# Optimization experiments

Hardware: AMD Instinct MI355X
Metric: run time of the kernel (lower is better)

The kernel has to match this reference:

```python
import jax, jax.numpy as jnp
import numpy as np

N_QUBITS = 12
DEPTH = 6
BATCH = 4096

# Wire 0 is the most-significant bit (PennyLane default.qubit convention).

def _rx(t):
    c = jnp.cos(t / 2).astype(jnp.complex64)
    s = (-1j * jnp.sin(t / 2)).astype(jnp.complex64)
    return jnp.stack([jnp.stack([c, s], -1), jnp.stack([s, c], -1)], -2)

def _ry(t):
    c = jnp.cos(t / 2).astype(jnp.complex64)
    s = jnp.sin(t / 2).astype(jnp.complex64)
    return jnp.stack([jnp.stack([c, -s], -1), jnp.stack([s, c], -1)], -2)

def _rz(t):
    em = jnp.exp(-1j * t.astype(jnp.complex64) / 2)
    ep = jnp.exp(1j * t.astype(jnp.complex64) / 2)
    z = jnp.zeros_like(em)
    return jnp.stack([jnp.stack([em, z], -1), jnp.stack([z, ep], -1)], -2)

def _apply_1q(state, gate, q, n):
    # state: (B, 2^n); gate: (2,2) shared or (B,2,2) batched
    B = state.shape[0]
    st = state.reshape(B, 1 << q, 2, 1 << (n - 1 - q))
    eq = 'ab,xlbr->xlar' if gate.ndim == 2 else 'xab,xlbr->xlar'
    return jnp.einsum(eq, gate, st).reshape(B, -1)

def _apply_cnot(state, c, n):
    # CNOT with control c, target c+1 (adjacent wires)
    B = state.shape[0]
    st = state.reshape(B, 1 << c, 2, 2, 1 << (n - 2 - c))
    st = jnp.concatenate([st[:, :, 0:1], st[:, :, 1:2, ::-1]], axis=2)
    return st.reshape(B, -1)

def _z_signs(n):
    idx = jnp.arange(1 << n)
    bits = (idx[None, :] >> (n - 1 - jnp.arange(n))[:, None]) & 1  # (n, 2^n)
    return (1.0 - 2.0 * bits).astype(jnp.float32)

def setup_inputs() -> dict:
    key = jax.random.key(0)
    k1, k2 = jax.random.split(key)
    x = jax.random.normal(k1, (BATCH, N_QUBITS), dtype=jnp.float32)
    params = jax.random.normal(k2, (DEPTH, N_QUBITS, 3), dtype=jnp.float32)
    return {"x": x, "params": params}

def reference(x, params):
    B, n = x.shape
    depth = params.shape[0]
    state = jnp.zeros((B, 1 << n), jnp.complex64).at[:, 0].set(1.0)
    # input encoding: batched RX per qubit
    for i in range(n):
        state = _apply_1q(state, _rx(x[:, i]), i, n)
    for d in range(depth):
        for i in range(n):
            state = _apply_1q(state, _ry(params[d, i, 0]), i, n)
            state = _apply_1q(state, _rz(params[d, i, 1]), i, n)
            state = _apply_1q(state, _rx(params[d, i, 2]), i, n)
        for i in range(n - 1):
            state = _apply_cnot(state, i, n)
    probs = state.real ** 2 + state.imag ** 2  # (B, 2^n)
    return probs @ _z_signs(n).T  # (B, n) Pauli-Z expvals
```

## Files before the change

kernel.cpp:

```cpp
#include <hip/hip_runtime.h>

#define NQ    12
#define DIM   4096
#define DEPTH 6
#define BLK   256
#define RJ    16


typedef float f32x2 __attribute__((ext_vector_type(2)));

__device__ __host__ __forceinline__ constexpr int sufxc(int v) {
  v ^= v >> 1; v ^= v >> 2; v ^= v >> 4; v ^= v >> 8; return v;
}
__device__ __host__ __forceinline__ constexpr int K1w(int j) { return (j << 4) ^ j; }
__device__ __host__ __forceinline__ constexpr int K2w(int j) { return j << 8; }
__device__ __host__ __forceinline__ constexpr int KCw(int j) {
  const int s4 = sufxc(j) & 15;
  const int p  = __builtin_popcount((unsigned)j) & 1;
  return (s4 << 8) | (p ? 0xF0 : 0);
}

__device__ __forceinline__ f32x2 pfma(f32x2 a, f32x2 b, f32x2 c) {
  return __builtin_elementwise_fma(a, b, c);
}

template <int B>
__device__ __forceinline__ void gate4(f32x2 (&amp)[RJ], float4 u0, float4 u1) {
  const f32x2 r00 = {u0.x, u0.x}, mi00 = {-u0.y, u0.y};
  const f32x2 r01 = {u0.z, u0.z}, mi01 = {-u0.w, u0.w};
  const f32x2 r10 = {u1.x, u1.x}, mi10 = {-u1.y, u1.y};
  const f32x2 r11 = {u1.z, u1.z}, mi11 = {-u1.w, u1.w};
#pragma unroll
  for (int m = 0; m < RJ / 2; ++m) {
    const int lo = m & ((1 << B) - 1);
    const int j0 = ((m >> B) << (B + 1)) | lo;
    const int j1 = j0 | (1 << B);
    const f32x2 a = amp[j0], b = amp[j1];
    const f32x2 ax = a.yx, bx = b.yx;
    f32x2 n0 = r00 * a;
    n0 = pfma(mi00, ax, n0);
    n0 = pfma(r01, b, n0);
    n0 = pfma(mi01, bx, n0);
    f32x2 n1 = r10 * a;
    n1 = pfma(mi10, ax, n1);
    n1 = pfma(r11, b, n1);
    n1 = pfma(mi11, bx, n1);
    amp[j0] = n0; amp[j1] = n1;
  }
}

__global__ __launch_bounds__(BLK) void qsim_kernel(const float* __restrict__ x,
                                                   const float* __restrict__ params,
                                                   float* __restrict__ out) {
  __shared__ f32x2 sm2[DIM];
  __shared__ float uTab[DEPTH * NQ * 8];

  const int T = threadIdx.x;
  const int b = blockIdx.x;

  if (T < DEPTH * NQ) {
    const float py = params[T * 3 + 0];
    const float pz = params[T * 3 + 1];
    const float px = params[T * 3 + 2];
    float sa, ca, sb, cb, sg, cg;
    __sincosf(py * 0.5f, &sa, &ca);
    __sincosf(pz * 0.5f, &sb, &cb);
    __sincosf(px * 0.5f, &sg, &cg);
    const float Ar = ca * cb, Ai = -ca * sb;
    const float Br = -sa * cb, Bi = sa * sb;
    const float Cr = sa * cb, Ci = sa * sb;
    const float Dr = ca * cb, Di = ca * sb;
    float* u = &uTab[T * 8];
    u[0] = cg * Ar + sg * Ci;   u[1] = cg * Ai - sg * Cr;
    u[2] = cg * Br + sg * Di;   u[3] = cg * Bi - sg * Dr;
    u[4] = sg * Ai + cg * Cr;   u[5] = -sg * Ar + cg * Ci;
    u[6] = sg * Bi + cg * Dr;   u[7] = -sg * Br + cg * Di;
  }

  f32x2 amp[RJ];
  {
    float cs[NQ], sn[NQ];
#pragma unroll
    for (int i = 0; i < NQ; ++i) __sincosf(x[b * NQ + i] * 0.5f, &sn[i], &cs[i]);
    float hm = 1.0f;
#pragma unroll
    for (int i = 0; i < 8; ++i) hm *= ((T >> (7 - i)) & 1) ? sn[i] : cs[i];
    float mag[RJ];
    mag[0] = hm;
#pragma unroll
    for (int bb = 0; bb < 4; ++bb) {
#pragma unroll
      for (int j = 0; j < (1 << bb); ++j) {
        mag[j | (1 << bb)] = mag[j] * sn[11 - bb];
        mag[j] = mag[j] * cs[11 - bb];
      }
    }
    const int pt = __popc(T);
#pragma unroll
    for (int j = 0; j < RJ; ++j) {
      const float m = mag[j];
      const int k = (pt + __popc(j)) & 3;
      const float rr = (k & 1) ? 0.0f : ((k & 2) ? -m : m);
      const float ii = (k & 1) ? ((k & 2) ? m : -m) : 0.0f;
      amp[j] = (f32x2){rr, ii};
    }
  }

  __syncthreads();

  const int A0w = (T << 4) ^ (T & 15);
  const int B0w = ((T >> 4) << 8) | (T & 15);
  const int C0w = T ^ ((T >> 4) & 15);
  const int CT  = sufxc(T) & 255;
  const int D0w = CT ^ ((CT >> 4) & 15);

#define SWEEP(D, WBASE)                                                       \
  {                                                                           \
    const float4* uv0 = (const float4*)&uTab[((D) * NQ + (WBASE)) * 8];       \
    gate4<0>(amp, uv0[0], uv0[1]);                                            \
    const float4* uv1 = (const float4*)&uTab[((D) * NQ + (WBASE) - 1) * 8];   \
    gate4<1>(amp, uv1[0], uv1[1]);                                            \
    const float4* uv2 = (const float4*)&uTab[((D) * NQ + (WBASE) - 2) * 8];   \
    gate4<2>(amp, uv2[0], uv2[1]);                                            \
    const float4* uv3 = (const float4*)&uTab[((D) * NQ + (WBASE) - 3) * 8];   \
    gate4<3>(amp, uv3[0], uv3[1]);                                            \
  }
#define ST_ALL(EXPR)                                                          \
  {                                                                           \
    _Pragma("unroll") for (int j = 0; j < RJ; ++j) { sm2[(EXPR)] = amp[j]; }  \
  }
#define LD_ALL(EXPR)                                                          \
  {                                                                           \
    _Pragma("unroll") for (int j = 0; j < RJ; ++j) { amp[j] = sm2[(EXPR)]; }  \
  }

#pragma unroll 1
  for (int d = 0; d < DEPTH; ++d) {
    SWEEP(d, 11)
    ST_ALL(A0w ^ j) __syncthreads();
    LD_ALL(B0w ^ K1w(j)) __syncthreads();
    SWEEP(d, 7)
    ST_ALL(B0w ^ K1w(j)) __syncthreads();
    LD_ALL(C0w ^ K2w(j)) __syncthreads();
    SWEEP(d, 3)
    ST_ALL(D0w ^ KCw(j)) __syncthreads();
    LD_ALL(A0w ^ j) __syncthreads();
  }
#undef SWEEP
#undef ST_ALL
#undef LD_ALL

  float tot = 0.f, s0 = 0.f, s1 = 0.f, s2 = 0.f, s3 = 0.f;
#pragma unroll
  for (int j = 0; j < RJ; ++j) {
    const float p = fmaf(amp[j].x, amp[j].x, amp[j].y * amp[j].y);
    tot += p;
    s0 += (j & 1) ? -p : p;
    s1 += (j & 2) ? -p : p;
    s2 += (j & 4) ? -p : p;
    s3 += (j & 8) ? -p : p;
  }
  float v[NQ];
#pragma unroll
  for (int w = 0; w < 8; ++w) v[w] = ((T >> (7 - w)) & 1) ? -tot : tot;
  v[8] = s3; v[9] = s2; v[10] = s1; v[11] = s0;
#pragma unroll
  for (int w = 0; w < NQ; ++w) {
#pragma unroll
    for (int o = 32; o > 0; o >>= 1) v[w] += __shfl_xor(v[w], o);
  }
  const int wv = T >> 6, lt = T & 63;
  float* smf = (float*)sm2;
  if (lt == 0) {
#pragma unroll
    for (int w = 0; w < NQ; ++w) smf[w * 4 + wv] = v[w];
  }
  __syncthreads();
  if (T < NQ) out[b * NQ + T] = (smf[T * 4 + 0] + smf[T * 4 + 1]) +
                                (smf[T * 4 + 2] + smf[T * 4 + 3]);
}

extern "C" void kernel_launch(void* const* d_in, const int* in_sizes, int n_in,
                              void* d_out, int out_size, void* d_ws, size_t ws_size,
                              hipStream_t stream) {
  const float* x      = (const float*)d_in[0];
  const float* params = (const float*)d_in[1];
  float* out          = (float*)d_out;
  const int B = in_sizes[0] / NQ;
  qsim_kernel<<<B, BLK, 0, stream>>>(x, params, out);
}
```

Baseline: 242.5 us.

## Precompute gate table in a prep kernel and drop intra-wave LDS barriers

Moves the fused RY·RZ·RX gate matrices into a separate one-block kernel that writes them to workspace. The main kernel now reads them with uniform global loads instead of rebuilding an LDS table in every block. It also removes the barriers around the first LDS exchange, which only moves data between lanes of the same 16-thread group inside one wavefront, and reorders the others so each depth needs three barriers instead of six. This relies on wavefront lockstep for the unsynchronised exchange and adds a second kernel launch.

```diff
diff --git a/kernel.cpp b/kernel.cpp
--- a/kernel.cpp
+++ b/kernel.cpp
@@ -49,33 +49,34 @@
   }
 }
 
+__global__ void gate_prep(const float* __restrict__ params, float* __restrict__ gt) {
+  const int T = threadIdx.x;
+  if (T >= DEPTH * NQ) return;
+  const float py = params[T * 3 + 0];
+  const float pz = params[T * 3 + 1];
+  const float px = params[T * 3 + 2];
+  float sa, ca, sb, cb, sg, cg;
+  __sincosf(py * 0.5f, &sa, &ca);
+  __sincosf(pz * 0.5f, &sb, &cb);
+  __sincosf(px * 0.5f, &sg, &cg);
+  const float Ar = ca * cb, Ai = -ca * sb;
+  const float Br = -sa * cb, Bi = sa * sb;
+  const float Cr = sa * cb, Ci = sa * sb;
+  const float Dr = ca * cb, Di = ca * sb;
+  float* u = &gt[T * 8];
+  u[0] = cg * Ar + sg * Ci;   u[1] = cg * Ai - sg * Cr;
+  u[2] = cg * Br + sg * Di;   u[3] = cg * Bi - sg * Dr;
+  u[4] = sg * Ai + cg * Cr;   u[5] = -sg * Ar + cg * Ci;
+  u[6] = sg * Bi + cg * Dr;   u[7] = -sg * Br + cg * Di;
+}
+
 __global__ __launch_bounds__(BLK) void qsim_kernel(const float* __restrict__ x,
-                                                   const float* __restrict__ params,
+                                                   const float* __restrict__ gt,
                                                    float* __restrict__ out) {
   __shared__ f32x2 sm2[DIM];
-  __shared__ float uTab[DEPTH * NQ * 8];
 
   const int T = threadIdx.x;
   const int b = blockIdx.x;
-
-  if (T < DEPTH * NQ) {
-    const float py = params[T * 3 + 0];
-    const float pz = params[T * 3 + 1];
-    const float px = params[T * 3 + 2];
-    float sa, ca, sb, cb, sg, cg;
-    __sincosf(py * 0.5f, &sa, &ca);
-    __sincosf(pz * 0.5f, &sb, &cb);
-    __sincosf(px * 0.5f, &sg, &cg);
-    const float Ar = ca * cb, Ai = -ca * sb;
-    const float Br = -sa * cb, Bi = sa * sb;
-    const float Cr = sa * cb, Ci = sa * sb;
-    const float Dr = ca * cb, Di = ca * sb;
-    float* u = &uTab[T * 8];
-    u[0] = cg * Ar + sg * Ci;   u[1] = cg * Ai - sg * Cr;
-    u[2] = cg * Br + sg * Di;   u[3] = cg * Bi - sg * Dr;
-    u[4] = sg * Ai + cg * Cr;   u[5] = -sg * Ar + cg * Ci;
-    u[6] = sg * Bi + cg * Dr;   u[7] = -sg * Br + cg * Di;
-  }
 
   f32x2 amp[RJ];
   {
@@ -106,8 +107,6 @@
     }
   }
 
-  __syncthreads();
-
   const int A0w = (T << 4) ^ (T & 15);
   const int B0w = ((T >> 4) << 8) | (T & 15);
   const int C0w = T ^ ((T >> 4) & 15);
@@ -116,13 +115,13 @@
 
 #define SWEEP(D, WBASE)                                                       \
   {                                                                           \
-    const float4* uv0 = (const float4*)&uTab[((D) * NQ + (WBASE)) * 8];       \
+    const float4* uv0 = (const float4*)&gt[((D) * NQ + (WBASE)) * 8];         \
     gate4<0>(amp, uv0[0], uv0[1]);                                            \
-    const float4* uv1 = (const float4*)&uTab[((D) * NQ + (WBASE) - 1) * 8];   \
+    const float4* uv1 = (const float4*)&gt[((D) * NQ + (WBASE) - 1) * 8];     \
     gate4<1>(amp, uv1[0], uv1[1]);                                            \
-    const float4* uv2 = (const float4*)&uTab[((D) * NQ + (WBASE) - 2) * 8];   \
+    const float4* uv2 = (const float4*)&gt[((D) * NQ + (WBASE) - 2) * 8];     \
     gate4<2>(amp, uv2[0], uv2[1]);                                            \
-    const float4* uv3 = (const float4*)&uTab[((D) * NQ + (WBASE) - 3) * 8];   \
+    const float4* uv3 = (const float4*)&gt[((D) * NQ + (WBASE) - 3) * 8];     \
     gate4<3>(amp, uv3[0], uv3[1]);                                            \
   }
 #define ST_ALL(EXPR)                                                          \
@@ -137,14 +136,17 @@
 #pragma unroll 1
   for (int d = 0; d < DEPTH; ++d) {
     SWEEP(d, 11)
-    ST_ALL(A0w ^ j) __syncthreads();
-    LD_ALL(B0w ^ K1w(j)) __syncthreads();
+    ST_ALL(A0w ^ j)
+    LD_ALL(B0w ^ K1w(j))
     SWEEP(d, 7)
-    ST_ALL(B0w ^ K1w(j)) __syncthreads();
-    LD_ALL(C0w ^ K2w(j)) __syncthreads();
+    ST_ALL(B0w ^ K1w(j))
+    __syncthreads();
+    LD_ALL(C0w ^ K2w(j))
     SWEEP(d, 3)
-    ST_ALL(D0w ^ KCw(j)) __syncthreads();
-    LD_ALL(A0w ^ j) __syncthreads();
+    __syncthreads();
+    ST_ALL(D0w ^ KCw(j))
+    __syncthreads();
+    LD_ALL(A0w ^ j)
   }
 #undef SWEEP
 #undef ST_ALL
@@ -169,6 +171,7 @@
 #pragma unroll
     for (int o = 32; o > 0; o >>= 1) v[w] += __shfl_xor(v[w], o);
   }
+  __syncthreads();
   const int wv = T >> 6, lt = T & 63;
   float* smf = (float*)sm2;
   if (lt == 0) {
@@ -186,6 +189,8 @@
   const float* x      = (const float*)d_in[0];
   const float* params = (const float*)d_in[1];
   float* out          = (float*)d_out;
+  float* gt           = (float*)d_ws;
   const int B = in_sizes[0] / NQ;
-  qsim_kernel<<<B, BLK, 0, stream>>>(x, params, out);
+  gate_prep<<<1, 128, 0, stream>>>(params, gt);
+  qsim_kernel<<<B, BLK, 0, stream>>>(x, gt, out);
 }
```

New measurement: 238.2 us. No clear change (-1.7%).
